# Kernel optimization log

Hardware: AMD Instinct MI355X
Metric: run time of the kernel (lower is better)

## Reference

```python
import jax, jax.numpy as jnp
import numpy as np

N_HEAD = 16
DROP_P = 0.1


def setup_inputs() -> dict:
    key = jax.random.key(0)
    ks = jax.random.split(key, 5)
    B, T, C = 2, 2048, 1024
    return {
        "x": jax.random.normal(ks[0], (B, T, C), dtype=jnp.float32),
        "w_attn": jax.random.normal(ks[1], (C, 3 * C), dtype=jnp.float32) * 0.02,
        "b_attn": jax.random.normal(ks[2], (3 * C,), dtype=jnp.float32) * 0.02,
        "w_proj": jax.random.normal(ks[3], (C, C), dtype=jnp.float32) * 0.02,
        "b_proj": jax.random.normal(ks[4], (C,), dtype=jnp.float32) * 0.02,
    }


def reference(x, w_attn, b_attn, w_proj, b_proj):
    B, T, C = x.shape
    H = N_HEAD
    D = C // H  # head dim
    qkv = x @ w_attn + b_attn                      # [B,T,3C]
    q, k, v = jnp.split(qkv, 3, axis=-1)
    # [B,T,C] -> [B,H,T,D]
    q = q.reshape(B, T, H, D).transpose(0, 2, 1, 3)
    k = k.reshape(B, T, H, D).transpose(0, 2, 1, 3)
    v = v.reshape(B, T, H, D).transpose(0, 2, 1, 3)
    scale = 1.0 / jnp.sqrt(jnp.float32(D))
    attn = jnp.einsum("bhqd,bhkd->bhqk", q, k) * scale  # [B,H,T,T]
    causal = jnp.tril(jnp.ones((T, T), dtype=bool))
    attn = jnp.where(causal[None, None], attn, jnp.float32(-jnp.inf))
    attn = jax.nn.softmax(attn, axis=-1)
    # dropout p=0.1 (training mode in original); deterministic fixed key here
    keep = jax.random.bernoulli(jax.random.key(42), 1.0 - DROP_P, attn.shape)
    attn = jnp.where(keep, attn / (1.0 - DROP_P), 0.0)
    out = jnp.einsum("bhqk,bhkd->bhqd", attn, v)   # [B,H,T,D]
    out = out.transpose(0, 2, 1, 3).reshape(B, T, C)
    return out @ w_proj + b_proj
```

## Files before the change

### kernel.cpp

```cpp
#include <hip/hip_runtime.h>
#include <hip/hip_bf16.h>
#include <stdint.h>
#include <math.h>

#define TSEQ   2048
#define NBATCH 2
#define NHEAD  16
#define HDIM   64
#define CDIM   1024

#define KEEP_THRESH 7549747u
#define QSC 0.18033688011112042f

typedef short  bf16x8 __attribute__((ext_vector_type(8)));
typedef float  f32x4  __attribute__((ext_vector_type(4)));

__device__ __forceinline__ uint32_t rotl32(uint32_t x, int r) {
    return __builtin_amdgcn_alignbit(x, x, 32 - r);
}

__device__ __forceinline__ uint32_t tf2x32_xor(uint32_t x0, uint32_t x1) {
    const uint32_t ka = 0u, kb = 42u;
    const uint32_t kc = ka ^ kb ^ 0x1BD11BDAu;
    x0 += ka; x1 += kb;
#define TFR(r) { x0 += x1; x1 = rotl32(x1, r); x1 ^= x0; }
    TFR(13) TFR(15) TFR(26) TFR(6)
    x0 += kb; x1 += kc + 1u;
    TFR(17) TFR(29) TFR(16) TFR(24)
    x0 += kc; x1 += ka + 2u;
    TFR(13) TFR(15) TFR(26) TFR(6)
    x0 += ka; x1 += kb + 3u;
    TFR(17) TFR(29) TFR(16) TFR(24)
    x0 += kb; x1 += kc + 4u;
    TFR(13) TFR(15) TFR(26) TFR(6)
    x0 += kc; x1 += ka + 5u;
#undef TFR
    return x0 ^ x1;
}

__device__ __forceinline__ bool tf_keep(uint32_t idx) {
    return (tf2x32_xor(0u, idx) >> 9) < KEEP_THRESH;
}

__device__ __forceinline__ ushort f2bf(float f) {
    __hip_bfloat16 h = __float2bfloat16(f);
    return *reinterpret_cast<ushort*>(&h);
}

__device__ __forceinline__ float bf2f(ushort u) {
    union { uint32_t i; float f; } c; c.i = ((uint32_t)u) << 16; return c.f;
}

__device__ __forceinline__ void async_copy16(void* lds, const void* g) {
    __builtin_amdgcn_global_load_lds(
        (const __attribute__((address_space(1))) unsigned int*)g,
        (__attribute__((address_space(3))) unsigned int*)lds, 16, 0, 0);
}

__global__ __launch_bounds__(256) void cvt_bf16(
    const float* __restrict__ src, ushort* __restrict__ dst, int n)
{
    int idx = (blockIdx.x * 256 + threadIdx.x) * 8;
    if (idx >= n) return;
    float4 a = *(const float4*)(src + idx);
    float4 b = *(const float4*)(src + idx + 4);
    ushort4 o1; o1.x = f2bf(a.x); o1.y = f2bf(a.y); o1.z = f2bf(a.z); o1.w = f2bf(a.w);
    ushort4 o2; o2.x = f2bf(b.x); o2.y = f2bf(b.y); o2.z = f2bf(b.z); o2.w = f2bf(b.w);
    *(ushort4*)(dst + idx) = o1;
    *(ushort4*)(dst + idx + 4) = o2;
}

__global__ __launch_bounds__(256) void transpose_cvt(
    const float* __restrict__ src, ushort* __restrict__ dst, int K, int N)
{
    __shared__ float t[32][33];
    const int n0 = blockIdx.x * 32, k0 = blockIdx.y * 32;
    const int i = threadIdx.x;
    {
        int k = i >> 3, n4 = (i & 7) * 4;
        float4 v = *(const float4*)(src + (size_t)(k0 + k) * N + n0 + n4);
        t[k][n4 + 0] = v.x; t[k][n4 + 1] = v.y; t[k][n4 + 2] = v.z; t[k][n4 + 3] = v.w;
    }
    __syncthreads();
    {
        int n = i >> 3, k4 = (i & 7) * 4;
        ushort4 o;
        o.x = f2bf(t[k4 + 0][n]); o.y = f2bf(t[k4 + 1][n]);
        o.z = f2bf(t[k4 + 2][n]); o.w = f2bf(t[k4 + 3][n]);
        *(ushort4*)(dst + (size_t)(n0 + n) * K + k0 + k4) = o;
    }
}

template<int MODE>
__global__ __launch_bounds__(256) void gemm_bf16(
    const ushort* __restrict__ A, const ushort* __restrict__ Bt,
    const float* __restrict__ bias,
    ushort* __restrict__ Q, ushort* __restrict__ Kq, ushort* __restrict__ V,
    float* __restrict__ Cf, int M, int N, int K)
{
    __shared__ ushort As[2][128 * 32];
    __shared__ ushort Bs[2][128 * 32];
    const int tid = threadIdx.x, lane = tid & 63, wid = tid >> 6;
    const int l15 = lane & 15, l4 = lane >> 4;
    const int wr = wid >> 1, wc = wid & 1;
    const int bn = blockIdx.x, bm = blockIdx.y;
    const int NTK = K >> 5;

    f32x4 acc[4][4];
#pragma unroll
    for (int m = 0; m < 4; ++m)
#pragma unroll
        for (int n = 0; n < 4; ++n) acc[m][n] = (f32x4){0.f, 0.f, 0.f, 0.f};

    auto stage = [&](int p, int k0) {
#pragma unroll
        for (int j = 0; j < 2; ++j) {
            const int rbase = wid * 32 + j * 16;
            const int row = rbase + (lane >> 2);
            const ushort* src = A + (size_t)(bm * 128 + row) * K + k0 + (lane & 3) * 8;
            async_copy16(&As[p][rbase * 32], src);
        }
#pragma unroll
        for (int j = 0; j < 2; ++j) {
            const int rbase = wid * 32 + j * 16;
            const int row = rbase + (lane >> 2);
            const ushort* src = Bt + (size_t)(bn * 128 + row) * K + k0 + (lane & 3) * 8;
            async_copy16(&Bs[p][rbase * 32], src);
        }
    };
    auto compute = [&](int p) {
        bf16x8 af[4], bf[4];
#pragma unroll
        for (int m = 0; m < 4; ++m)
            af[m] = *(const bf16x8*)&As[p][(wr * 64 + m * 16 + l15) * 32 + l4 * 8];
#pragma unroll
        for (int n = 0; n < 4; ++n)
            bf[n] = *(const bf16x8*)&Bs[p][(wc * 64 + n * 16 + l15) * 32 + l4 * 8];
#pragma unroll
        for (int m = 0; m < 4; ++m)
#pragma unroll
            for (int n = 0; n < 4; ++n)
                acc[m][n] = __builtin_amdgcn_mfma_f32_16x16x32_bf16(af[m], bf[n], acc[m][n], 0, 0, 0);
    };

    stage(0, 0);
    __syncthreads();
    for (int t = 0; t < NTK; ++t) {
        const int p = t & 1;
        if (t + 1 < NTK) stage(p ^ 1, (t + 1) << 5);
        compute(p);
        __syncthreads();
    }

    const int colbase = bn * 128 + wc * 64;
    const int rowbase = bm * 128 + wr * 64;
    if (MODE == 0) {
#pragma unroll
        for (int n = 0; n < 4; ++n) {
            const int col = colbase + n * 16 + l15;
            const float bv = bias[col];
#pragma unroll
            for (int m = 0; m < 4; ++m)
#pragma unroll
                for (int r = 0; r < 4; ++r) {
                    const int row = rowbase + m * 16 + l4 * 4 + r;
                    Cf[(size_t)row * N + col] = acc[m][n][r] + bv;
                }
        }
    } else {
#pragma unroll
        for (int n = 0; n < 4; ++n) {
            const int col = colbase + n * 16 + l15;
            const int which = col >> 10, cc = col & 1023;
            const int hh = cc >> 6, dd = cc & 63;
            const float bv = bias[col];
            const float sc = (which == 0) ? QSC : 1.0f;
#pragma unroll
            for (int m = 0; m < 4; ++m)
#pragma unroll
                for (int r = 0; r < 4; ++r) {
                    const int row = rowbase + m * 16 + l4 * 4 + r;
                    const int bb = row >> 11, tt = row & 2047;
                    const ushort val = f2bf((acc[m][n][r] + bv) * sc);
                    if (which == 0)
                        Q[(((size_t)(bb * NHEAD + hh)) * TSEQ + tt) * HDIM + dd] = val;
                    else if (which == 1)
                        Kq[(((size_t)(bb * NHEAD + hh)) * TSEQ + tt) * HDIM + dd] = val;
                    else
                        V[(((size_t)(bb * NHEAD + hh)) * HDIM + dd) * TSEQ + tt] = val;
                }
        }
    }
}

__global__ __launch_bounds__(256) void attn_fwd_mfma(
    const ushort* __restrict__ Qb, const ushort* __restrict__ Kb,
    const ushort* __restrict__ VbT,
    ushort* __restrict__ Ap, float* __restrict__ mp, float* __restrict__ lp)
{
    __shared__ ushort Ks[2][64 * 64];
    __shared__ ushort Vt[2][64 * 64];
    __shared__ ushort Ps[64 * 64];
    const int tid = threadIdx.x;
    const int lane = tid & 63;
    const int wid = tid >> 6;
    const int l15 = lane & 15, l4 = lane >> 4;
    const int pair = blockIdx.x >> 1, half = blockIdx.x & 1;
    const int h = blockIdx.y, b = blockIdx.z;
    const int hb = b * NHEAD + h;
    const size_t headoff = (size_t)hb * TSEQ * HDIM;
    const ushort* Qg = Qb + headoff;
    const ushort* Kg = Kb + headoff;
    const ushort* Vg = VbT + headoff;

    auto stage = [&](int p, int kt) {
        const ushort* Kt = Kg + (size_t)(kt * 64) * HDIM;
        const ushort* Vt0 = Vg + kt * 64;
#pragma unroll
        for (int c = 0; c < 2; ++c) {
            const int rbase = wid * 16 + c * 8;
            const int row = rbase + (lane >> 3);
            const ushort* srcK = Kt + row * 64 + (((lane & 7) * 8) ^ ((row & 7) << 3));
            async_copy16(&Ks[p][rbase * 64], srcK);
            const ushort* srcV = Vt0 + (size_t)row * TSEQ + (((lane & 7) * 8) ^ ((row & 7) << 3));
            async_copy16(&Vt[p][rbase * 64], srcV);
        }
    };

    const int swq = (l15 & 7) << 3;
    const int prow = wid * 16 + l15;

    for (int pass = 0; pass < 2; ++pass) {
        const int qt = pass ? (TSEQ / 64 - 1) - pair : pair;
        const int ntk = qt + 1;
        const int kb = half ? (ntk + 1) >> 1 : 0;
        const int ke = half ? ntk : (ntk + 1) >> 1;
        const int pidx = (hb * 32 + qt) * 2 + half;
        const int tilerow = wid * 16 + l15;
        ushort* arow = Ap + (size_t)pidx * 4096 + tilerow * 64;

        if (kb >= ke) {
#pragma unroll
            for (int dt = 0; dt < 4; ++dt) {
                ushort4 z; z.x = z.y = z.z = z.w = 0;
                *(ushort4*)&arow[dt * 16 + l4 * 4] = z;
            }
            if (l4 == 0) { mp[pidx * 64 + tilerow] = -INFINITY; lp[pidx * 64 + tilerow] = 0.f; }
            continue;
        }

        const int qglob = qt * 64 + tilerow;
        bf16x8 qf0, qf1;
        {
            const ushort* qrow = Qg + (size_t)qglob * HDIM;
            qf0 = *(const bf16x8*)(qrow + l4 * 8);
            qf1 = *(const bf16x8*)(qrow + 32 + l4 * 8);
        }

        f32x4 oacc[4];
#pragma unroll
        for (int i = 0; i < 4; ++i) oacc[i] = (f32x4){0.f, 0.f, 0.f, 0.f};
        float mi = -INFINITY, li = 0.f;
        const uint32_t rowbase = ((uint32_t)hb * TSEQ + (uint32_t)qglob) * TSEQ;

        stage(0, kb);
        __syncthreads();

        for (int kt = kb; kt < ke; ++kt) {
            const int p = (kt - kb) & 1;
            if (kt + 1 < ke) stage(p ^ 1, kt + 1);

            f32x4 s4[4];
#pragma unroll
            for (int ct = 0; ct < 4; ++ct) {
                const int krow = ct * 16 + l15;
                const int sw = (krow & 7) << 3;
                bf16x8 kf0 = *(const bf16x8*)&Ks[p][krow * 64 + ((l4 * 8) ^ sw)];
                bf16x8 kf1 = *(const bf16x8*)&Ks[p][krow * 64 + ((l4 * 8 + 32) ^ sw)];
                f32x4 a = {0.f, 0.f, 0.f, 0.f};
                a = __builtin_amdgcn_mfma_f32_16x16x32_bf16(kf0, qf0, a, 0, 0, 0);
                a = __builtin_amdgcn_mfma_f32_16x16x32_bf16(kf1, qf1, a, 0, 0, 0);
                s4[ct] = a;
            }

            const int kb0 = kt * 64;
            float ev[4][4];
            float mx = -INFINITY;
            if (kt == qt) {
#pragma unroll
                for (int ct = 0; ct < 4; ++ct)
#pragma unroll
                    for (int r = 0; r < 4; ++r) {
                        const int kglob = kb0 + ct * 16 + l4 * 4 + r;
                        ev[ct][r] = (kglob <= qglob) ? s4[ct][r] : -INFINITY;
                        mx = fmaxf(mx, ev[ct][r]);
                    }
            } else {
#pragma unroll
                for (int ct = 0; ct < 4; ++ct)
#pragma unroll
                    for (int r = 0; r < 4; ++r) {
                        ev[ct][r] = s4[ct][r];
                        mx = fmaxf(mx, ev[ct][r]);
                    }
            }
            mx = fmaxf(mx, __shfl_xor(mx, 16));
            mx = fmaxf(mx, __shfl_xor(mx, 32));
            const float mnew = fmaxf(mi, mx);
            const float alpha = exp2f(mi - mnew);
            mi = mnew;
            float rs = 0.f;
#pragma unroll
            for (int ct = 0; ct < 4; ++ct)
#pragma unroll
                for (int r = 0; r < 4; ++r) {
                    ev[ct][r] = exp2f(ev[ct][r] - mnew);
                    rs += ev[ct][r];
                }
            rs += __shfl_xor(rs, 16);
            rs += __shfl_xor(rs, 32);
            li = li * alpha + rs;
#pragma unroll
            for (int dt = 0; dt < 4; ++dt) {
                oacc[dt][0] *= alpha; oacc[dt][1] *= alpha;
                oacc[dt][2] *= alpha; oacc[dt][3] *= alpha;
            }

            const uint32_t idx0 = rowbase + (uint32_t)kb0;
#pragma unroll
            for (int ct = 0; ct < 4; ++ct) {
                const uint32_t kk = idx0 + (uint32_t)(ct * 16 + l4 * 4);
                ushort4 pk;
                pk.x = f2bf(tf_keep(kk + 0u) ? ev[ct][0] : 0.f);
                pk.y = f2bf(tf_keep(kk + 1u) ? ev[ct][1] : 0.f);
                pk.z = f2bf(tf_keep(kk + 2u) ? ev[ct][2] : 0.f);
                pk.w = f2bf(tf_keep(kk + 3u) ? ev[ct][3] : 0.f);
                *(ushort4*)&Ps[prow * 64 + ((ct * 16 + l4 * 4) ^ swq)] = pk;
            }

            bf16x8 pf0 = *(const bf16x8*)&Ps[prow * 64 + ((l4 * 8) ^ swq)];
            bf16x8 pf1 = *(const bf16x8*)&Ps[prow * 64 + ((l4 * 8 + 32) ^ swq)];
#pragma unroll
            for (int dt = 0; dt < 4; ++dt) {
                const int drow = dt * 16 + l15;
                const int swv = (drow & 7) << 3;
                bf16x8 vf0 = *(const bf16x8*)&Vt[p][drow * 64 + ((l4 * 8) ^ swv)];
                bf16x8 vf1 = *(const bf16x8*)&Vt[p][drow * 64 + ((l4 * 8 + 32) ^ swv)];
                oacc[dt] = __builtin_amdgcn_mfma_f32_16x16x32_bf16(vf0, pf0, oacc[dt], 0, 0, 0);
                oacc[dt] = __builtin_amdgcn_mfma_f32_16x16x32_bf16(vf1, pf1, oacc[dt], 0, 0, 0);
            }
            __syncthreads();
        }

#pragma unroll
        for (int dt = 0; dt < 4; ++dt) {
            ushort4 o;
            o.x = f2bf(oacc[dt][0]); o.y = f2bf(oacc[dt][1]);
            o.z = f2bf(oacc[dt][2]); o.w = f2bf(oacc[dt][3]);
            *(ushort4*)&arow[dt * 16 + l4 * 4] = o;
        }
        if (l4 == 0) { mp[pidx * 64 + tilerow] = mi; lp[pidx * 64 + tilerow] = li; }
    }
}

__global__ __launch_bounds__(256) void attn_merge(
    const ushort* __restrict__ Ap, const float* __restrict__ mp,
    const float* __restrict__ lp, ushort* __restrict__ AO)
{
    const int gidx = blockIdx.x * 16 + (threadIdx.x >> 4);
    const int hb = gidx >> 11;
    const int q  = gidx & 2047;
    const int qt = q >> 6, row = q & 63;
    const int sub = (threadIdx.x & 15) * 4;
    const int pidx0 = (hb * 32 + qt) * 2;
    const int pr = pidx0 * 64 + row;
    const float m0 = mp[pr], m1 = mp[pr + 64];
    const float l0 = lp[pr], l1 = lp[pr + 64];
    const float m  = fmaxf(m0, m1);
    const float w0 = exp2f(m0 - m), w1 = exp2f(m1 - m);
    const float inv = 1.0f / ((l0 * w0 + l1 * w1) * 0.9f);
    const float s0 = w0 * inv, s1 = w1 * inv;
    ushort4 a0 = *(const ushort4*)&Ap[(size_t)pidx0 * 4096 + row * 64 + sub];
    ushort4 a1 = *(const ushort4*)&Ap[(size_t)(pidx0 + 1) * 4096 + row * 64 + sub];
    const int b = hb >> 4, h = hb & 15;
    ushort* orow = AO + ((size_t)(b * TSEQ + q)) * CDIM + h * HDIM + sub;
    ushort4 o;
    o.x = f2bf(bf2f(a0.x) * s0 + bf2f(a1.x) * s1);
    o.y = f2bf(bf2f(a0.y) * s0 + bf2f(a1.y) * s1);
    o.z = f2bf(bf2f(a0.z) * s0 + bf2f(a1.z) * s1);
    o.w = f2bf(bf2f(a0.w) * s0 + bf2f(a1.w) * s1);
    *(ushort4*)orow = o;
}

extern "C" void kernel_launch(void* const* d_in, const int* in_sizes, int n_in,
                              void* d_out, int out_size, void* d_ws, size_t ws_size,
                              hipStream_t stream)
{
    const float* x      = (const float*)d_in[0];
    const float* w_attn = (const float*)d_in[1];
    const float* b_attn = (const float*)d_in[2];
    const float* w_proj = (const float*)d_in[3];
    const float* b_proj = (const float*)d_in[4];
    float* out = (float*)d_out;

    const size_t NH = (size_t)NBATCH * NHEAD * TSEQ * HDIM;
    ushort* Qb  = (ushort*)d_ws;
    ushort* Kb  = Qb + NH;
    ushort* VbT = Kb + NH;
    ushort* AO  = VbT + NH;
    ushort* xb  = AO + NH;
    ushort* wTa = xb + NH;
    ushort* wTp = wTa + (size_t)3072 * 1024;
    float*  mp  = (float*)(wTp + (size_t)1024 * 1024);
    float*  lp  = mp + (size_t)2048 * 64;

    ushort* Aparts = (ushort*)d_out;

    cvt_bf16<<<2048, 256, 0, stream>>>(x, xb, 4096 * 1024);
    transpose_cvt<<<dim3(96, 32), 256, 0, stream>>>(w_attn, wTa, 1024, 3072);
    transpose_cvt<<<dim3(32, 32), 256, 0, stream>>>(w_proj, wTp, 1024, 1024);

    gemm_bf16<1><<<dim3(24, 32), 256, 0, stream>>>(
        xb, wTa, b_attn, Qb, Kb, VbT, nullptr, 4096, 3072, 1024);

    attn_fwd_mfma<<<dim3(32, NHEAD, NBATCH), 256, 0, stream>>>(
        Qb, Kb, VbT, Aparts, mp, lp);

    attn_merge<<<4096, 256, 0, stream>>>(Aparts, mp, lp, AO);

    gemm_bf16<0><<<dim3(8, 32), 256, 0, stream>>>(
        AO, wTp, b_proj, nullptr, nullptr, nullptr, out, 4096, 1024, 1024);
}
```

Measured before the change: 247.1 us.

## Use packed bf16 converts, raw exp2, lazy rescale, and simpler dropout compare

Replaces per-element software float-to-bf16 conversion with the hardware packed v_cvt_pk_bf16_f32 instruction across all kernels, and swaps exp2f for the raw v_exp_f32 instruction. In attention, the online-softmax rescale of the accumulator is skipped when no lane's row max increased, and the max reduction is rebalanced into a tree. The dropout keep test compares the full 32-bit hash to a single threshold instead of shifting first. These cut VALU work in the attention inner loop and the epilogues. The risks are slight numerical differences from the raw exp instruction, and a wave-divergent branch per tile.

```diff
diff --git a/kernel.cpp b/kernel.cpp
--- a/kernel.cpp
+++ b/kernel.cpp
@@ -9,11 +9,18 @@
 #define HDIM   64
 #define CDIM   1024
 
-#define KEEP_THRESH 7549747u
+#define KEEP_LIMIT 3865470464u
 #define QSC 0.18033688011112042f
 
 typedef short  bf16x8 __attribute__((ext_vector_type(8)));
 typedef float  f32x4  __attribute__((ext_vector_type(4)));
+
+__device__ __forceinline__ float fast_exp2(float x) {
+    float r; asm("v_exp_f32 %0, %1" : "=v"(r) : "v"(x)); return r;
+}
+__device__ __forceinline__ uint32_t cvt_pk_bf16(float a, float b) {
+    uint32_t r; asm("v_cvt_pk_bf16_f32 %0, %1, %2" : "=v"(r) : "v"(a), "v"(b)); return r;
+}
 
 __device__ __forceinline__ uint32_t rotl32(uint32_t x, int r) {
     return __builtin_amdgcn_alignbit(x, x, 32 - r);
@@ -39,12 +46,7 @@
 }
 
 __device__ __forceinline__ bool tf_keep(uint32_t idx) {
-    return (tf2x32_xor(0u, idx) >> 9) < KEEP_THRESH;
-}
-
-__device__ __forceinline__ ushort f2bf(float f) {
-    __hip_bfloat16 h = __float2bfloat16(f);
-    return *reinterpret_cast<ushort*>(&h);
+    return tf2x32_xor(0u, idx) < KEEP_LIMIT;
 }
 
 __device__ __forceinline__ float bf2f(ushort u) {
@@ -64,10 +66,10 @@
     if (idx >= n) return;
     float4 a = *(const float4*)(src + idx);
     float4 b = *(const float4*)(src + idx + 4);
-    ushort4 o1; o1.x = f2bf(a.x); o1.y = f2bf(a.y); o1.z = f2bf(a.z); o1.w = f2bf(a.w);
-    ushort4 o2; o2.x = f2bf(b.x); o2.y = f2bf(b.y); o2.z = f2bf(b.z); o2.w = f2bf(b.w);
-    *(ushort4*)(dst + idx) = o1;
-    *(ushort4*)(dst + idx + 4) = o2;
+    uint4 o;
+    o.x = cvt_pk_bf16(a.x, a.y); o.y = cvt_pk_bf16(a.z, a.w);
+    o.z = cvt_pk_bf16(b.x, b.y); o.w = cvt_pk_bf16(b.z, b.w);
+    *(uint4*)(dst + idx) = o;
 }
 
 __global__ __launch_bounds__(256) void transpose_cvt(
@@ -84,10 +86,10 @@
     __syncthreads();
     {
         int n = i >> 3, k4 = (i & 7) * 4;
-        ushort4 o;
-        o.x = f2bf(t[k4 + 0][n]); o.y = f2bf(t[k4 + 1][n]);
-        o.z = f2bf(t[k4 + 2][n]); o.w = f2bf(t[k4 + 3][n]);
-        *(ushort4*)(dst + (size_t)(n0 + n) * K + k0 + k4) = o;
+        uint2 o;
+        o.x = cvt_pk_bf16(t[k4 + 0][n], t[k4 + 1][n]);
+        o.y = cvt_pk_bf16(t[k4 + 2][n], t[k4 + 3][n]);
+        *(uint2*)(dst + (size_t)(n0 + n) * K + k0 + k4) = o;
     }
 }
 
@@ -176,19 +178,24 @@
             const float bv = bias[col];
             const float sc = (which == 0) ? QSC : 1.0f;
 #pragma unroll
-            for (int m = 0; m < 4; ++m)
+            for (int m = 0; m < 4; ++m) {
+                float v0 = (acc[m][n][0] + bv) * sc, v1 = (acc[m][n][1] + bv) * sc;
+                float v2 = (acc[m][n][2] + bv) * sc, v3 = (acc[m][n][3] + bv) * sc;
+                uint32_t pk01 = cvt_pk_bf16(v0, v1), pk23 = cvt_pk_bf16(v2, v3);
+                ushort vals[4] = { (ushort)pk01, (ushort)(pk01 >> 16),
+                                   (ushort)pk23, (ushort)(pk23 >> 16) };
 #pragma unroll
                 for (int r = 0; r < 4; ++r) {
                     const int row = rowbase + m * 16 + l4 * 4 + r;
                     const int bb = row >> 11, tt = row & 2047;
-                    const ushort val = f2bf((acc[m][n][r] + bv) * sc);
                     if (which == 0)
-                        Q[(((size_t)(bb * NHEAD + hh)) * TSEQ + tt) * HDIM + dd] = val;
+                        Q[(((size_t)(bb * NHEAD + hh)) * TSEQ + tt) * HDIM + dd] = vals[r];
                     else if (which == 1)
-                        Kq[(((size_t)(bb * NHEAD + hh)) * TSEQ + tt) * HDIM + dd] = val;
+                        Kq[(((size_t)(bb * NHEAD + hh)) * TSEQ + tt) * HDIM + dd] = vals[r];
                     else
-                        V[(((size_t)(bb * NHEAD + hh)) * HDIM + dd) * TSEQ + tt] = val;
+                        V[(((size_t)(bb * NHEAD + hh)) * HDIM + dd) * TSEQ + tt] = vals[r];
                 }
+            }
         }
     }
 }
@@ -285,7 +292,6 @@
 
             const int kb0 = kt * 64;
             float ev[4][4];
-            float mx = -INFINITY;
             if (kt == qt) {
 #pragma unroll
                 for (int ct = 0; ct < 4; ++ct)
@@ -293,49 +299,62 @@
                     for (int r = 0; r < 4; ++r) {
                         const int kglob = kb0 + ct * 16 + l4 * 4 + r;
                         ev[ct][r] = (kglob <= qglob) ? s4[ct][r] : -INFINITY;
-                        mx = fmaxf(mx, ev[ct][r]);
                     }
             } else {
 #pragma unroll
                 for (int ct = 0; ct < 4; ++ct)
 #pragma unroll
-                    for (int r = 0; r < 4; ++r) {
-                        ev[ct][r] = s4[ct][r];
-                        mx = fmaxf(mx, ev[ct][r]);
-                    }
+                    for (int r = 0; r < 4; ++r) ev[ct][r] = s4[ct][r];
+            }
+            float mx;
+            {
+                float t0 = fmaxf(fmaxf(ev[0][0], ev[0][1]), ev[0][2]);
+                float t1 = fmaxf(fmaxf(ev[0][3], ev[1][0]), ev[1][1]);
+                float t2 = fmaxf(fmaxf(ev[1][2], ev[1][3]), ev[2][0]);
+                float t3 = fmaxf(fmaxf(ev[2][1], ev[2][2]), ev[2][3]);
+                float t4 = fmaxf(fmaxf(ev[3][0], ev[3][1]), ev[3][2]);
+                float t5 = fmaxf(fmaxf(t0, t1), ev[3][3]);
+                float t6 = fmaxf(fmaxf(t2, t3), t4);
+                mx = fmaxf(t5, t6);
             }
             mx = fmaxf(mx, __shfl_xor(mx, 16));
             mx = fmaxf(mx, __shfl_xor(mx, 32));
-            const float mnew = fmaxf(mi, mx);
-            const float alpha = exp2f(mi - mnew);
-            mi = mnew;
+
+            if (__any(mx > mi)) {
+                const float mnew = fmaxf(mi, mx);
+                const float alpha = fast_exp2(mi - mnew);
+                mi = mnew;
+                li *= alpha;
+#pragma unroll
+                for (int dt = 0; dt < 4; ++dt) {
+                    oacc[dt][0] *= alpha; oacc[dt][1] *= alpha;
+                    oacc[dt][2] *= alpha; oacc[dt][3] *= alpha;
+                }
+            }
             float rs = 0.f;
 #pragma unroll
             for (int ct = 0; ct < 4; ++ct)
 #pragma unroll
                 for (int r = 0; r < 4; ++r) {
-                    ev[ct][r] = exp2f(ev[ct][r] - mnew);
+                    ev[ct][r] = fast_exp2(ev[ct][r] - mi);
                     rs += ev[ct][r];
                 }
             rs += __shfl_xor(rs, 16);
             rs += __shfl_xor(rs, 32);
-            li = li * alpha + rs;
-#pragma unroll
-            for (int dt = 0; dt < 4; ++dt) {
-                oacc[dt][0] *= alpha; oacc[dt][1] *= alpha;
-                oacc[dt][2] *= alpha; oacc[dt][3] *= alpha;
-            }
+            li += rs;
 
             const uint32_t idx0 = rowbase + (uint32_t)kb0;
 #pragma unroll
             for (int ct = 0; ct < 4; ++ct) {
                 const uint32_t kk = idx0 + (uint32_t)(ct * 16 + l4 * 4);
-                ushort4 pk;
-                pk.x = f2bf(tf_keep(kk + 0u) ? ev[ct][0] : 0.f);
-                pk.y = f2bf(tf_keep(kk + 1u) ? ev[ct][1] : 0.f);
-                pk.z = f2bf(tf_keep(kk + 2u) ? ev[ct][2] : 0.f);
-                pk.w = f2bf(tf_keep(kk + 3u) ? ev[ct][3] : 0.f);
-                *(ushort4*)&Ps[prow * 64 + ((ct * 16 + l4 * 4) ^ swq)] = pk;
+                const float p0 = tf_keep(kk + 0u) ? ev[ct][0] : 0.f;
+                const float p1 = tf_keep(kk + 1u) ? ev[ct][1] : 0.f;
+                const float p2 = tf_keep(kk + 2u) ? ev[ct][2] : 0.f;
+                const float p3 = tf_keep(kk + 3u) ? ev[ct][3] : 0.f;
+                uint2 pk;
+                pk.x = cvt_pk_bf16(p0, p1);
+                pk.y = cvt_pk_bf16(p2, p3);
+                *(uint2*)&Ps[prow * 64 + ((ct * 16 + l4 * 4) ^ swq)] = pk;
             }
 
             bf16x8 pf0 = *(const bf16x8*)&Ps[prow * 64 + ((l4 * 8) ^ swq)];
@@ -354,10 +373,10 @@
 
 #pragma unroll
         for (int dt = 0; dt < 4; ++dt) {
-            ushort4 o;
-            o.x = f2bf(oacc[dt][0]); o.y = f2bf(oacc[dt][1]);
-            o.z = f2bf(oacc[dt][2]); o.w = f2bf(oacc[dt][3]);
-            *(ushort4*)&arow[dt * 16 + l4 * 4] = o;
+            uint2 o;
+            o.x = cvt_pk_bf16(oacc[dt][0], oacc[dt][1]);
+            o.y = cvt_pk_bf16(oacc[dt][2], oacc[dt][3]);
+            *(uint2*)&arow[dt * 16 + l4 * 4] = o;
         }
         if (l4 == 0) { mp[pidx * 64 + tilerow] = mi; lp[pidx * 64 + tilerow] = li; }
     }
@@ -377,19 +396,19 @@
     const float m0 = mp[pr], m1 = mp[pr + 64];
     const float l0 = lp[pr], l1 = lp[pr + 64];
     const float m  = fmaxf(m0, m1);
-    const float w0 = exp2f(m0 - m), w1 = exp2f(m1 - m);
+    const float w0 = fast_exp2(m0 - m), w1 = fast_exp2(m1 - m);
     const float inv = 1.0f / ((l0 * w0 + l1 * w1) * 0.9f);
     const float s0 = w0 * inv, s1 = w1 * inv;
     ushort4 a0 = *(const ushort4*)&Ap[(size_t)pidx0 * 4096 + row * 64 + sub];
     ushort4 a1 = *(const ushort4*)&Ap[(size_t)(pidx0 + 1) * 4096 + row * 64 + sub];
     const int b = hb >> 4, h = hb & 15;
     ushort* orow = AO + ((size_t)(b * TSEQ + q)) * CDIM + h * HDIM + sub;
-    ushort4 o;
-    o.x = f2bf(bf2f(a0.x) * s0 + bf2f(a1.x) * s1);
-    o.y = f2bf(bf2f(a0.y) * s0 + bf2f(a1.y) * s1);
-    o.z = f2bf(bf2f(a0.z) * s0 + bf2f(a1.z) * s1);
-    o.w = f2bf(bf2f(a0.w) * s0 + bf2f(a1.w) * s1);
-    *(ushort4*)orow = o;
+    uint2 o;
+    o.x = cvt_pk_bf16(bf2f(a0.x) * s0 + bf2f(a1.x) * s1,
+                      bf2f(a0.y) * s0 + bf2f(a1.y) * s1);
+    o.y = cvt_pk_bf16(bf2f(a0.z) * s0 + bf2f(a1.z) * s1,
+                      bf2f(a0.w) * s0 + bf2f(a1.w) * s1);
+    *(uint2*)orow = o;
 }
 
 extern "C" void kernel_launch(void* const* d_in, const int* in_sizes, int n_in,
```

After: 236.0 us. -4.5%, faster.
